# Kernel tuning notes

Hardware: AMD Instinct MI355X
Metric: run time of the kernel (lower is better)

## Reference

```python
import jax, jax.numpy as jnp
import numpy as np
from jax import lax

B, P, S, H, F, V, O = 32, 24, 48, 512, 64, 50000, 16
EPS = 1e-5


def _lstm_scan(inputs, Wih, Whh, b):
    # inputs: [T, B, D]; PyTorch gate order i, f, g, o
    def step(carry, xt):
        h, c = carry
        g = xt @ Wih.T + h @ Whh.T + b
        i, f, gg, o = jnp.split(g, 4, axis=-1)
        c = jax.nn.sigmoid(f) * c + jax.nn.sigmoid(i) * jnp.tanh(gg)
        h = jax.nn.sigmoid(o) * jnp.tanh(c)
        return (h, c), h
    b_ = inputs.shape[1]
    h0 = jnp.zeros((b_, Whh.shape[1]), inputs.dtype)
    _, hs = lax.scan(step, (h0, h0), inputs)
    return hs


def setup_inputs() -> dict:
    key = jax.random.key(0)
    ks = jax.random.split(key, 16)
    x = jax.random.randint(ks[0], (B, P, S), 0, V)
    lens = jnp.sort(jax.random.randint(ks[1], (B,), 1, P + 1))[::-1]
    lens = lens.at[0].set(P)  # pack_padded: sorted desc, max len == P
    tok_len = jax.random.randint(ks[2], (B, P), 1, S + 1)
    tok_len = tok_len * (jnp.arange(P)[None, :] < lens[:, None])
    x_mask = jnp.arange(S)[None, None, :] >= tok_len[:, :, None]  # True = pad
    x_feature = jax.random.normal(ks[3], (B, P, S, F), dtype=jnp.float32)
    emb = jax.random.normal(ks[4], (V, H), dtype=jnp.float32) * 0.02
    w_attn = jax.random.normal(ks[5], (H,), dtype=jnp.float32) * 0.02
    b_attn = jnp.zeros((), jnp.float32)
    D = H + F
    s = 1.0 / np.sqrt(H)
    u = lambda k, sh: jax.random.uniform(k, sh, jnp.float32, -s, s)
    Wih_f, Whh_f = u(ks[6], (4 * H, D)), u(ks[7], (4 * H, H))
    bih_f, bhh_f = u(ks[8], (4 * H,)), u(ks[9], (4 * H,))
    Wih_b, Whh_b = u(ks[10], (4 * H, D)), u(ks[11], (4 * H, H))
    bih_b, bhh_b = u(ks[12], (4 * H,)), u(ks[13], (4 * H,))
    Wfc = u(ks[14], (O, 2 * H))
    bfc = jnp.zeros((O,), jnp.float32)
    gamma = jnp.ones((O,), jnp.float32)
    beta = jnp.zeros((O,), jnp.float32)
    return {"x": x, "x_mask": x_mask, "x_feature": x_feature,
            "sentences_len": lens, "clause": 0, "cls": 0,
            "emb": emb, "w_attn": w_attn, "b_attn": b_attn,
            "Wih_f": Wih_f, "Whh_f": Whh_f, "bih_f": bih_f, "bhh_f": bhh_f,
            "Wih_b": Wih_b, "Whh_b": Whh_b, "bih_b": bih_b, "bhh_b": bhh_b,
            "Wfc": Wfc, "bfc": bfc, "gamma": gamma, "beta": beta}


def reference(x, x_mask, x_feature, sentences_len, clause, cls,
              emb, w_attn, b_attn,
              Wih_f, Whh_f, bih_f, bhh_f,
              Wih_b, Whh_b, bih_b, bhh_b,
              Wfc, bfc, gamma, beta):
    # --- per-sentence embed + linear self-attention + masked sum pooling ---
    e = emb[x]                                             # [B,P,S,H]
    scores = jnp.einsum('bpsh,h->bps', e, w_attn) + b_attn  # [B,P,S]
    scores = jnp.where(x_mask, -1e30, scores)
    alpha = jax.nn.softmax(scores, axis=-1)
    alpha = jnp.where(x_mask, 0.0, alpha)                  # zeros empty sents; relu(softmax)=softmax
    valid = (~x_mask).astype(e.dtype)
    weighted = e * alpha[..., None]
    cat = jnp.concatenate([weighted, x_feature], axis=-1) * valid[..., None]
    rep = cat.sum(axis=2)                                  # [B,P,H+F]
    seq = jnp.transpose(rep, (1, 0, 2))                    # time-major [P,B,H+F]

    # --- packed bidirectional LSTM (per-sequence reversal for bwd dir) ---
    t = jnp.arange(P)[:, None]                             # [P,1]
    lens = sentences_len[None, :]                          # [1,B]
    valid_t = (t < lens)                                   # [P,B]
    h_fwd = _lstm_scan(seq, Wih_f, Whh_f, bih_f + bhh_f)
    rev_idx = jnp.clip(lens - 1 - t, 0)                    # [P,B]
    rev_in = jnp.take_along_axis(seq, rev_idx[..., None], axis=0)
    h_bwd_rev = _lstm_scan(rev_in, Wih_b, Whh_b, bih_b + bhh_b)
    h_bwd = jnp.take_along_axis(h_bwd_rev, rev_idx[..., None], axis=0)
    out_seq = jnp.concatenate([h_fwd, h_bwd], axis=-1) * valid_t[..., None]  # pad_packed zeros

    # --- tail: last timestep, fc, train-mode BN, relu, log_softmax(dim=0) ---
    last = out_seq[-1]                                     # [B,2H]
    z = jnp.reshape(last.T, (B, 2 * H))                    # faithful transpose+view quirk
    y = z @ Wfc.T + bfc                                    # [B,O]
    mean = y.mean(axis=0)
    var = y.var(axis=0)                                    # biased, as torch BN normalization
    y = gamma * (y - mean) / jnp.sqrt(var + EPS) + beta
    y = jax.nn.relu(y)
    return jax.nn.log_softmax(y, axis=0)
```

## Files before the change

### kernel.cpp

```cpp
#include <hip/hip_runtime.h>
#include <math.h>

#define BB_ 32
#define PP_ 24
#define SS_ 48
#define HH_ 512
#define FF_ 64
#define DD_ 576
#define G4_ 2048

typedef __attribute__((ext_vector_type(8))) short short8;
typedef __attribute__((ext_vector_type(4))) float f32x4;

__device__ __forceinline__ float sigf(float x) { return 1.f / (1.f + expf(-x)); }

__device__ __forceinline__ unsigned short f2bf(float f) {
    unsigned int u = __float_as_uint(f);
    u += 0x7FFFu + ((u >> 16) & 1u);
    return (unsigned short)(u >> 16);
}

__global__ void detect_mask_kernel(const unsigned int* __restrict__ m,
                                   int* __restrict__ mode)
{
    __shared__ int s_u8, s_f32;
    int tid = threadIdx.x;
    if (tid == 0) { s_u8 = 0; s_f32 = 0; }
    __syncthreads();
    int u8 = 0, f32 = 0;
    for (int i = tid; i < 9216; i += 256) {
        unsigned int w = m[i];
        if (w == 0x3F800000u) f32 = 1;
        else if (w > 1u) u8 = 1;
    }
    if (u8) s_u8 = 1;
    if (f32) s_f32 = 1;
    __syncthreads();
    if (tid == 0) *mode = s_f32 ? 2 : (s_u8 ? 1 : 0);
}

__global__ void attn_rep_kernel(const int* __restrict__ x,
                                const void* __restrict__ x_mask,
                                const int* __restrict__ mode_p,
                                const float* __restrict__ x_feature,
                                const float* __restrict__ emb,
                                const float* __restrict__ w_attn,
                                const float* __restrict__ b_attn,
                                float* __restrict__ seq)
{
    int bp = blockIdx.x;
    int b = bp / PP_, p = bp % PP_;
    int tid = threadIdx.x;
    __shared__ float wattn_s[HH_];
    __shared__ float sc_s[SS_];
    __shared__ float alpha_s[SS_];
    __shared__ int idx_s[SS_];
    __shared__ unsigned char msk_s[SS_];
    int mode = *mode_p;
    wattn_s[tid] = w_attn[tid];
    wattn_s[tid + 256] = w_attn[tid + 256];
    if (tid < SS_) {
        size_t i = (size_t)bp * SS_ + tid;
        idx_s[tid] = x[i];
        unsigned char mv;
        if (mode == 1)      mv = ((const unsigned char*)x_mask)[i];
        else if (mode == 2) mv = (((const float*)x_mask)[i] != 0.f);
        else                mv = (((const int*)x_mask)[i] != 0);
        msk_s[tid] = mv;
    }
    __syncthreads();
    int wave = tid >> 6, lane = tid & 63;
    for (int s = wave; s < SS_; s += 4) {
        const float* er = emb + (size_t)idx_s[s] * HH_;
        float acc = 0.f;
        #pragma unroll
        for (int j = 0; j < 8; ++j) {
            int d = lane * 8 + j;
            acc += er[d] * wattn_s[d];
        }
        #pragma unroll
        for (int off = 32; off > 0; off >>= 1) acc += __shfl_down(acc, off, 64);
        if (lane == 0) sc_s[s] = acc + b_attn[0];
    }
    __syncthreads();
    if (tid == 0) {
        float m = -3.4e38f;
        for (int s = 0; s < SS_; ++s) if (!msk_s[s] && sc_s[s] > m) m = sc_s[s];
        float sum = 0.f;
        for (int s = 0; s < SS_; ++s) {
            float a = 0.f;
            if (!msk_s[s]) { a = expf(sc_s[s] - m); sum += a; }
            alpha_s[s] = a;
        }
        float inv = (sum > 0.f) ? (1.f / sum) : 0.f;
        for (int s = 0; s < SS_; ++s) alpha_s[s] *= inv;
    }
    __syncthreads();
    float acc0 = 0.f, acc1 = 0.f;
    for (int s = 0; s < SS_; ++s) {
        float a = alpha_s[s];
        if (a != 0.f) {
            const float* er = emb + (size_t)idx_s[s] * HH_;
            acc0 += a * er[tid];
            acc1 += a * er[tid + 256];
        }
    }
    float* orow = seq + ((size_t)p * BB_ + b) * DD_;
    orow[tid] = acc0;
    orow[tid + 256] = acc1;
    if (tid < FF_) {
        float acc2 = 0.f;
        for (int s = 0; s < SS_; ++s)
            if (!msk_s[s]) acc2 += x_feature[((size_t)bp * SS_ + s) * FF_ + tid];
        orow[HH_ + tid] = acc2;
    }
}

__global__ void init2_kernel(float* __restrict__ A0, float* __restrict__ cb)
{
    int i = blockIdx.x * 256 + threadIdx.x;
    if (i < 8192) A0[i] = 0.f;
    cb[i] = 0.f;
}

__global__ void cvt_bf16_kernel(const float* __restrict__ s,
                                unsigned short* __restrict__ d, int n4)
{
    int i = blockIdx.x * 256 + threadIdx.x;
    if (i >= n4) return;
    float4 v = ((const float4*)s)[i];
    ushort4 o;
    o.x = f2bf(v.x); o.y = f2bf(v.y); o.z = f2bf(v.z); o.w = f2bf(v.w);
    ((ushort4*)d)[i] = o;
}

__global__ void __launch_bounds__(256) in_gates_mfma_kernel(
        const float* __restrict__ A,
        const unsigned short* __restrict__ Wbf,
        const float* __restrict__ bih,
        const float* __restrict__ bhh,
        float* __restrict__ Cout)
{
    int tid = threadIdx.x, lane = tid & 63, w = tid >> 6;
    int m0 = blockIdx.y * 16;
    int nb = blockIdx.x * 128 + w * 32;
    int c = lane & 15, q = lane >> 4;
    const float* Ap = A + (size_t)(m0 + c) * DD_ + q * 8;
    const unsigned short* Bp0 = Wbf + (size_t)(nb + c) * DD_ + q * 8;
    const unsigned short* Bp1 = Bp0 + 16 * DD_;
    f32x4 acc0 = {0.f, 0.f, 0.f, 0.f}, acc1 = {0.f, 0.f, 0.f, 0.f};
    for (int k = 0; k < DD_; k += 32) {
        float4 alo = *(const float4*)(Ap + k);
        float4 ahi = *(const float4*)(Ap + k + 4);
        short8 a;
        a[0] = (short)f2bf(alo.x); a[1] = (short)f2bf(alo.y);
        a[2] = (short)f2bf(alo.z); a[3] = (short)f2bf(alo.w);
        a[4] = (short)f2bf(ahi.x); a[5] = (short)f2bf(ahi.y);
        a[6] = (short)f2bf(ahi.z); a[7] = (short)f2bf(ahi.w);
        short8 b0 = *(const short8*)(Bp0 + k);
        short8 b1 = *(const short8*)(Bp1 + k);
        acc0 = __builtin_amdgcn_mfma_f32_16x16x32_bf16(a, b0, acc0, 0, 0, 0);
        acc1 = __builtin_amdgcn_mfma_f32_16x16x32_bf16(a, b1, acc1, 0, 0, 0);
    }
    #pragma unroll
    for (int r = 0; r < 4; ++r) {
        int m = m0 + q * 4 + r;
        int n0 = nb + c, n1 = nb + 16 + c;
        Cout[(size_t)m * G4_ + n0] = acc0[r] + bih[n0] + bhh[n0];
        Cout[(size_t)m * G4_ + n1] = acc1[r] + bih[n1] + bhh[n1];
    }
}

__global__ void __launch_bounds__(256) bwd_last2_kernel(const float* __restrict__ seq,
        const int* __restrict__ lens,
        const float* __restrict__ Wih_b,
        const float* __restrict__ bih_b,
        const float* __restrict__ bhh_b,
        float* __restrict__ hb)
{
    __shared__ float xsT[DD_ * 33];
    __shared__ int pl[BB_];
    int tid = threadIdx.x;
    if (tid < BB_) pl[tid] = lens[tid] - 1;
    __syncthreads();
    for (int idx = tid; idx < BB_ * DD_; idx += 256) {
        int b2 = idx / DD_;
        int k = idx - b2 * DD_;
        xsT[k * 33 + b2] = seq[((size_t)pl[b2] * BB_ + b2) * DD_ + k];
    }
    __syncthreads();
    int b = tid & 31, ul = tid >> 5;
    int u = blockIdx.x * 8 + ul;
    const float* wi = Wih_b + (size_t)u * DD_;
    const float* wg = Wih_b + (size_t)(2 * HH_ + u) * DD_;
    const float* wo = Wih_b + (size_t)(3 * HH_ + u) * DD_;
    float gi = 0.f, gg = 0.f, go = 0.f;
    #pragma unroll 4
    for (int k = 0; k < DD_; k += 4) {
        float4 w1 = *(const float4*)(wi + k);
        float4 w2 = *(const float4*)(wg + k);
        float4 w3 = *(const float4*)(wo + k);
        float x0 = xsT[(k + 0) * 33 + b];
        float x1 = xsT[(k + 1) * 33 + b];
        float x2 = xsT[(k + 2) * 33 + b];
        float x3 = xsT[(k + 3) * 33 + b];
        gi += w1.x * x0 + w1.y * x1 + w1.z * x2 + w1.w * x3;
        gg += w2.x * x0 + w2.y * x1 + w2.z * x2 + w2.w * x3;
        go += w3.x * x0 + w3.y * x1 + w3.z * x2 + w3.w * x3;
    }
    gi += bih_b[u] + bhh_b[u];
    gg += bih_b[2 * HH_ + u] + bhh_b[2 * HH_ + u];
    go += bih_b[3 * HH_ + u] + bhh_b[3 * HH_ + u];
    float cc = sigf(gi) * tanhf(gg);
    hb[(size_t)b * HH_ + u] = sigf(go) * tanhf(cc);
}

__global__ void whh_frag_kernel(const float* __restrict__ Whh,
                                unsigned short* __restrict__ Bf)
{
    int idx = blockIdx.x * 256 + threadIdx.x;
    int lane = idx & 63;
    int ks = (idx >> 6) & 15;
    int ti = (idx >> 10) & 1;
    int nb = idx >> 11;
    int c = lane & 15, q = lane >> 4;
    int nrow = (ti * 2 + (c >> 3)) * HH_ + nb * 8 + (c & 7);
    int k0 = ks * 32 + q * 8;
    const float* src = Whh + (size_t)nrow * HH_ + k0;
    unsigned int w0 = (unsigned int)f2bf(src[0]) | ((unsigned int)f2bf(src[1]) << 16);
    unsigned int w1 = (unsigned int)f2bf(src[2]) | ((unsigned int)f2bf(src[3]) << 16);
    unsigned int w2 = (unsigned int)f2bf(src[4]) | ((unsigned int)f2bf(src[5]) << 16);
    unsigned int w3 = (unsigned int)f2bf(src[6]) | ((unsigned int)f2bf(src[7]) << 16);
    uint4 v = make_uint4(w0, w1, w2, w3);
    *(uint4*)(Bf + (size_t)idx * 8) = v;
}

__global__ void __launch_bounds__(256) lstm_mfma_kernel(
        const unsigned short* __restrict__ Afrag,
        unsigned short* __restrict__ AfragN,
        float* __restrict__ cbuf,
        float* __restrict__ hbuf,
        const float* __restrict__ Ain_t,
        const unsigned short* __restrict__ Bfrag)
{
    __shared__ float gl[32 * 33];
    int tid = threadIdx.x;
    int lane = tid & 63;
    int wv = tid >> 6;
    int mt = wv & 1, ti = wv >> 1;
    int nb = blockIdx.x;
    const short8* Ap = (const short8*)Afrag + (size_t)(mt * 16) * 64 + lane;
    const short8* Bp = (const short8*)Bfrag + (((size_t)nb * 2 + ti) * 16) * 64 + lane;
    short8 a[16], bfr[16];
    #pragma unroll
    for (int ks = 0; ks < 16; ++ks) { a[ks] = Ap[ks * 64]; bfr[ks] = Bp[ks * 64]; }
    f32x4 acc = {0.f, 0.f, 0.f, 0.f};
    #pragma unroll
    for (int ks = 0; ks < 16; ++ks)
        acc = __builtin_amdgcn_mfma_f32_16x16x32_bf16(a[ks], bfr[ks], acc, 0, 0, 0);
    int c = lane & 15, q = lane >> 4;
    int g = ti * 2 + (c >> 3), ul = c & 7;
    #pragma unroll
    for (int r = 0; r < 4; ++r) {
        int bb = mt * 16 + q * 4 + r;
        float v = acc[r] + Ain_t[(size_t)bb * G4_ + g * HH_ + nb * 8 + ul];
        v = (g == 2) ? tanhf(v) : sigf(v);
        gl[(g * 8 + ul) * 33 + bb] = v;
    }
    __syncthreads();
    int b2 = tid >> 3, u2 = tid & 7;
    float iv = gl[(0  + u2) * 33 + b2];
    float fv = gl[(8  + u2) * 33 + b2];
    float gv = gl[(16 + u2) * 33 + b2];
    float ov = gl[(24 + u2) * 33 + b2];
    int ug = nb * 8 + u2;
    size_t ci = (size_t)b2 * HH_ + ug;
    float cold = cbuf[ci];
    float cn = fv * cold + iv * gv;
    cbuf[ci] = cn;
    float h = ov * tanhf(cn);
    hbuf[ci] = h;
    int ks2 = ug >> 5, q2 = (ug >> 3) & 3, j2 = ug & 7;
    int lane2 = (b2 & 15) + 16 * q2;
    AfragN[(((size_t)(b2 >> 4) * 16 + ks2) * 64 + lane2) * 8 + j2] = f2bf(h);
}

__global__ void __launch_bounds__(256) fc_head_kernel(const float* __restrict__ hfwd,
        const float* __restrict__ hbwd, const int* __restrict__ lens,
        const float* __restrict__ Wfc, const float* __restrict__ bfc,
        float* __restrict__ yws)
{
    __shared__ float tile[32][33];
    __shared__ float part[16][17];
    int i = blockIdx.x;
    int tid = threadIdx.x;
    const float* src = (i < 16 ? hfwd : hbwd) + (size_t)(i & 15) * 32;
    int bb = tid >> 5, q = tid & 31;
    #pragma unroll
    for (int h = 0; h < 4; ++h) {
        int bi = bb + h * 8;
        float v = src[(size_t)bi * HH_ + q];
        tile[bi][q] = (lens[bi] == PP_) ? v : 0.f;
    }
    __syncthreads();
    int o = tid >> 4, s = tid & 15;
    const float* w = Wfc + (size_t)o * 1024;
    float acc = 0.f;
    #pragma unroll
    for (int qq = 0; qq < 32; ++qq) {
        acc += tile[s][qq]      * w[qq * 32 + s];
        acc += tile[s + 16][qq] * w[qq * 32 + s + 16];
    }
    part[o][s] = acc;
    __syncthreads();
    if (tid < 16) {
        float sum = bfc[tid];
        #pragma unroll
        for (int ss = 0; ss < 16; ++ss) sum += part[tid][ss];
        yws[i * 16 + tid] = sum;
    }
}

__global__ void __launch_bounds__(512) head_final_kernel(const float* __restrict__ yws,
        const float* __restrict__ gamma, const float* __restrict__ beta,
        float* __restrict__ out)
{
    __shared__ float ys[16][33];
    __shared__ float cstat[16];
    int tid = threadIdx.x;
    int i = tid >> 4, o = tid & 15;
    ys[o][i] = yws[tid];
    __syncthreads();
    if (tid < 16) {
        float mean = 0.f;
        for (int ii = 0; ii < 32; ++ii) mean += ys[tid][ii];
        mean *= (1.f / 32.f);
        float var = 0.f;
        for (int ii = 0; ii < 32; ++ii) { float d = ys[tid][ii] - mean; var += d * d; }
        var *= (1.f / 32.f);
        float inv = 1.f / sqrtf(var + 1e-5f);
        float g = gamma[tid], bt = beta[tid];
        float mx = -3.4e38f;
        for (int ii = 0; ii < 32; ++ii) {
            float v = g * (ys[tid][ii] - mean) * inv + bt;
            v = fmaxf(v, 0.f);
            ys[tid][ii] = v;
            mx = fmaxf(mx, v);
        }
        float s = 0.f;
        for (int ii = 0; ii < 32; ++ii) s += expf(ys[tid][ii] - mx);
        cstat[tid] = mx + logf(s);
    }
    __syncthreads();
    out[tid] = ys[o][i] - cstat[o];
}

extern "C" void kernel_launch(void* const* d_in, const int* in_sizes, int n_in,
                              void* d_out, int out_size, void* d_ws, size_t ws_size,
                              hipStream_t stream) {
    const int* x            = (const int*)d_in[0];
    const void* xm          = d_in[1];
    const float* x_feature  = (const float*)d_in[2];
    const int* lens         = (const int*)d_in[3];
    const float* emb    = (const float*)d_in[6];
    const float* w_attn = (const float*)d_in[7];
    const float* b_attn = (const float*)d_in[8];
    const float* Wih_f  = (const float*)d_in[9];
    const float* Whh_f  = (const float*)d_in[10];
    const float* bih_f  = (const float*)d_in[11];
    const float* bhh_f  = (const float*)d_in[12];
    const float* Wih_b  = (const float*)d_in[13];
    const float* bih_b  = (const float*)d_in[15];
    const float* bhh_b  = (const float*)d_in[16];
    const float* Wfc    = (const float*)d_in[17];
    const float* bfc    = (const float*)d_in[18];
    const float* gamma  = (const float*)d_in[19];
    const float* beta   = (const float*)d_in[20];

    float* ws    = (float*)d_ws;
    float* seq   = ws;
    float* Ain   = seq + (size_t)PP_ * BB_ * DD_;
    float* hb    = Ain + (size_t)PP_ * BB_ * G4_;
    float* hbuf  = hb + (size_t)BB_ * HH_;
    float* cbuf  = hbuf + (size_t)BB_ * HH_;
    float* AfA   = cbuf + (size_t)BB_ * HH_;
    float* AfB   = AfA + 8192;
    float* Bfrag = AfB + 8192;
    float* Wbf   = Bfrag + 524288;
    float* yws   = Wbf + 589824;
    int*  mflag  = (int*)(yws + 512);

    float* outp = (float*)d_out;

    detect_mask_kernel<<<dim3(1), dim3(256), 0, stream>>>(
        (const unsigned int*)xm, mflag);
    whh_frag_kernel<<<dim3(512), dim3(256), 0, stream>>>(
        Whh_f, (unsigned short*)Bfrag);
    cvt_bf16_kernel<<<dim3(1152), dim3(256), 0, stream>>>(
        Wih_f, (unsigned short*)Wbf, 294912);
    attn_rep_kernel<<<dim3(BB_ * PP_), dim3(256), 0, stream>>>(
        x, xm, mflag, x_feature, emb, w_attn, b_attn, seq);
    init2_kernel<<<dim3(64), dim3(256), 0, stream>>>(AfA, cbuf);
    in_gates_mfma_kernel<<<dim3(16, 48), dim3(256), 0, stream>>>(
        seq, (const unsigned short*)Wbf, bih_f, bhh_f, Ain);
    bwd_last2_kernel<<<dim3(64), dim3(256), 0, stream>>>(
        seq, lens, Wih_b, bih_b, bhh_b, hb);
    for (int t = 0; t < PP_; ++t) {
        const unsigned short* Asrc = (const unsigned short*)((t & 1) ? AfB : AfA);
        unsigned short* Adst       = (unsigned short*)((t & 1) ? AfA : AfB);
        lstm_mfma_kernel<<<dim3(64), dim3(256), 0, stream>>>(
            Asrc, Adst, cbuf, hbuf, Ain + (size_t)t * BB_ * G4_,
            (const unsigned short*)Bfrag);
    }
    fc_head_kernel<<<dim3(32), dim3(256), 0, stream>>>(
        hbuf, hb, lens, Wfc, bfc, yws);
    head_final_kernel<<<dim3(1), dim3(512), 0, stream>>>(
        yws, gamma, beta, outp);
}
```

Measured before the change: 457.7 us.

## Persist LSTM recurrence in one kernel with flag barriers and fuse prep/head kernels

```diff
diff --git a/kernel.cpp b/kernel.cpp
--- a/kernel.cpp
+++ b/kernel.cpp
@@ -20,45 +20,77 @@
     return (unsigned short)(u >> 16);
 }
 
-__global__ void detect_mask_kernel(const unsigned int* __restrict__ m,
-                                   int* __restrict__ mode)
-{
-    __shared__ int s_u8, s_f32;
-    int tid = threadIdx.x;
-    if (tid == 0) { s_u8 = 0; s_f32 = 0; }
-    __syncthreads();
-    int u8 = 0, f32 = 0;
-    for (int i = tid; i < 9216; i += 256) {
-        unsigned int w = m[i];
-        if (w == 0x3F800000u) f32 = 1;
-        else if (w > 1u) u8 = 1;
-    }
-    if (u8) s_u8 = 1;
-    if (f32) s_f32 = 1;
-    __syncthreads();
-    if (tid == 0) *mode = s_f32 ? 2 : (s_u8 ? 1 : 0);
-}
-
-__global__ void attn_rep_kernel(const int* __restrict__ x,
-                                const void* __restrict__ x_mask,
-                                const int* __restrict__ mode_p,
-                                const float* __restrict__ x_feature,
-                                const float* __restrict__ emb,
-                                const float* __restrict__ w_attn,
-                                const float* __restrict__ b_attn,
-                                float* __restrict__ seq)
-{
+__global__ void __launch_bounds__(256) prep_kernel(
+        const float* __restrict__ Whh, unsigned short* __restrict__ Bf,
+        const float* __restrict__ Wih, unsigned short* __restrict__ Wbf,
+        float* __restrict__ AfA,
+        const unsigned int* __restrict__ maskw, int* __restrict__ mode,
+        int* __restrict__ flags)
+{
+    int blk = blockIdx.x, tid = threadIdx.x;
+    if (blk < 512) {
+        int idx = blk * 256 + tid;
+        int lane = idx & 63;
+        int ks = (idx >> 6) & 15;
+        int ti = (idx >> 10) & 1;
+        int nb = idx >> 11;
+        int c = lane & 15, q = lane >> 4;
+        int nrow = (ti * 2 + (c >> 3)) * HH_ + nb * 8 + (c & 7);
+        int k0 = ks * 32 + q * 8;
+        const float* src = Whh + (size_t)nrow * HH_ + k0;
+        unsigned int w0 = (unsigned int)f2bf(src[0]) | ((unsigned int)f2bf(src[1]) << 16);
+        unsigned int w1 = (unsigned int)f2bf(src[2]) | ((unsigned int)f2bf(src[3]) << 16);
+        unsigned int w2 = (unsigned int)f2bf(src[4]) | ((unsigned int)f2bf(src[5]) << 16);
+        unsigned int w3 = (unsigned int)f2bf(src[6]) | ((unsigned int)f2bf(src[7]) << 16);
+        *(uint4*)(Bf + (size_t)idx * 8) = make_uint4(w0, w1, w2, w3);
+    } else if (blk < 1664) {
+        int i = (blk - 512) * 256 + tid;
+        float4 v = ((const float4*)Wih)[i];
+        ushort4 o;
+        o.x = f2bf(v.x); o.y = f2bf(v.y); o.z = f2bf(v.z); o.w = f2bf(v.w);
+        ((ushort4*)Wbf)[i] = o;
+    } else if (blk < 1728) {
+        int idx = (blk - 1664) * 256 + tid;
+        if (idx < 8192) AfA[idx] = 0.f;
+    } else {
+        __shared__ int s_u8, s_f32;
+        if (tid == 0) { s_u8 = 0; s_f32 = 0; }
+        __syncthreads();
+        int u8 = 0, f32 = 0;
+        for (int i = tid; i < 9216; i += 256) {
+            unsigned int w = maskw[i];
+            if (w == 0x3F800000u) f32 = 1;
+            else if (w > 1u) u8 = 1;
+        }
+        if (u8) s_u8 = 1;
+        if (f32) s_f32 = 1;
+        if (tid < 64) flags[tid] = 0;
+        __syncthreads();
+        if (tid == 0) *mode = s_f32 ? 2 : (s_u8 ? 1 : 0);
+    }
+}
+
+__global__ void __launch_bounds__(256) attn2_kernel(
+        const int* __restrict__ x,
+        const void* __restrict__ x_mask,
+        const int* __restrict__ mode_p,
+        const float* __restrict__ x_feature,
+        const float* __restrict__ emb,
+        const float* __restrict__ w_attn,
+        const float* __restrict__ b_attn,
+        float* __restrict__ seq)
+{
+    __shared__ float4 es4[SS_ * 128];
+    __shared__ float sc_s[SS_], alpha_s[SS_], vld_s[SS_];
+    __shared__ int idx_s[SS_];
+    __shared__ unsigned char msk_s[SS_];
+    float* esf = (float*)es4;
     int bp = blockIdx.x;
     int b = bp / PP_, p = bp % PP_;
     int tid = threadIdx.x;
-    __shared__ float wattn_s[HH_];
-    __shared__ float sc_s[SS_];
-    __shared__ float alpha_s[SS_];
-    __shared__ int idx_s[SS_];
-    __shared__ unsigned char msk_s[SS_];
+    int wave = tid >> 6, lane = tid & 63;
     int mode = *mode_p;
-    wattn_s[tid] = w_attn[tid];
-    wattn_s[tid + 256] = w_attn[tid + 256];
+    float bscal = b_attn[0];
     if (tid < SS_) {
         size_t i = (size_t)bp * SS_ + tid;
         idx_s[tid] = x[i];
@@ -67,20 +99,25 @@
         else if (mode == 2) mv = (((const float*)x_mask)[i] != 0.f);
         else                mv = (((const int*)x_mask)[i] != 0);
         msk_s[tid] = mv;
-    }
-    __syncthreads();
-    int wave = tid >> 6, lane = tid & 63;
+        vld_s[tid] = mv ? 0.f : 1.f;
+    }
+    __syncthreads();
+    for (int i = wave; i < 2 * SS_; i += 4) {
+        int s = i >> 1, part = i & 1;
+        const float4* er = (const float4*)(emb + (size_t)idx_s[s] * HH_);
+        es4[s * 128 + part * 64 + lane] = er[part * 64 + lane];
+    }
+    __syncthreads();
+    float4 wa0 = ((const float4*)w_attn)[lane];
+    float4 wa1 = ((const float4*)w_attn)[64 + lane];
     for (int s = wave; s < SS_; s += 4) {
-        const float* er = emb + (size_t)idx_s[s] * HH_;
-        float acc = 0.f;
-        #pragma unroll
-        for (int j = 0; j < 8; ++j) {
-            int d = lane * 8 + j;
-            acc += er[d] * wattn_s[d];
-        }
+        float4 v0 = es4[s * 128 + lane];
+        float4 v1 = es4[s * 128 + 64 + lane];
+        float acc = v0.x * wa0.x + v0.y * wa0.y + v0.z * wa0.z + v0.w * wa0.w
+                  + v1.x * wa1.x + v1.y * wa1.y + v1.z * wa1.z + v1.w * wa1.w;
         #pragma unroll
         for (int off = 32; off > 0; off >>= 1) acc += __shfl_down(acc, off, 64);
-        if (lane == 0) sc_s[s] = acc + b_attn[0];
+        if (lane == 0) sc_s[s] = acc + bscal;
     }
     __syncthreads();
     if (tid == 0) {
@@ -97,41 +134,21 @@
     }
     __syncthreads();
     float acc0 = 0.f, acc1 = 0.f;
+    #pragma unroll 8
     for (int s = 0; s < SS_; ++s) {
-        float a = alpha_s[s];
-        if (a != 0.f) {
-            const float* er = emb + (size_t)idx_s[s] * HH_;
-            acc0 += a * er[tid];
-            acc1 += a * er[tid + 256];
-        }
+        float al = alpha_s[s];
+        acc0 += al * esf[s * 512 + tid];
+        acc1 += al * esf[s * 512 + 256 + tid];
     }
     float* orow = seq + ((size_t)p * BB_ + b) * DD_;
     orow[tid] = acc0;
     orow[tid + 256] = acc1;
     if (tid < FF_) {
-        float acc2 = 0.f;
+        float accF = 0.f;
         for (int s = 0; s < SS_; ++s)
-            if (!msk_s[s]) acc2 += x_feature[((size_t)bp * SS_ + s) * FF_ + tid];
-        orow[HH_ + tid] = acc2;
-    }
-}
-
-__global__ void init2_kernel(float* __restrict__ A0, float* __restrict__ cb)
-{
-    int i = blockIdx.x * 256 + threadIdx.x;
-    if (i < 8192) A0[i] = 0.f;
-    cb[i] = 0.f;
-}
-
-__global__ void cvt_bf16_kernel(const float* __restrict__ s,
-                                unsigned short* __restrict__ d, int n4)
-{
-    int i = blockIdx.x * 256 + threadIdx.x;
-    if (i >= n4) return;
-    float4 v = ((const float4*)s)[i];
-    ushort4 o;
-    o.x = f2bf(v.x); o.y = f2bf(v.y); o.z = f2bf(v.z); o.w = f2bf(v.w);
-    ((ushort4*)d)[i] = o;
+            accF += vld_s[s] * x_feature[((size_t)bp * SS_ + s) * FF_ + tid];
+        orow[HH_ + tid] = accF;
+    }
 }
 
 __global__ void __launch_bounds__(256) in_gates_mfma_kernel(
@@ -215,121 +232,117 @@
     hb[(size_t)b * HH_ + u] = sigf(go) * tanhf(cc);
 }
 
-__global__ void whh_frag_kernel(const float* __restrict__ Whh,
-                                unsigned short* __restrict__ Bf)
-{
-    int idx = blockIdx.x * 256 + threadIdx.x;
-    int lane = idx & 63;
-    int ks = (idx >> 6) & 15;
-    int ti = (idx >> 10) & 1;
-    int nb = idx >> 11;
-    int c = lane & 15, q = lane >> 4;
-    int nrow = (ti * 2 + (c >> 3)) * HH_ + nb * 8 + (c & 7);
-    int k0 = ks * 32 + q * 8;
-    const float* src = Whh + (size_t)nrow * HH_ + k0;
-    unsigned int w0 = (unsigned int)f2bf(src[0]) | ((unsigned int)f2bf(src[1]) << 16);
-    unsigned int w1 = (unsigned int)f2bf(src[2]) | ((unsigned int)f2bf(src[3]) << 16);
-    unsigned int w2 = (unsigned int)f2bf(src[4]) | ((unsigned int)f2bf(src[5]) << 16);
-    unsigned int w3 = (unsigned int)f2bf(src[6]) | ((unsigned int)f2bf(src[7]) << 16);
-    uint4 v = make_uint4(w0, w1, w2, w3);
-    *(uint4*)(Bf + (size_t)idx * 8) = v;
-}
-
-__global__ void __launch_bounds__(256) lstm_mfma_kernel(
-        const unsigned short* __restrict__ Afrag,
-        unsigned short* __restrict__ AfragN,
-        float* __restrict__ cbuf,
-        float* __restrict__ hbuf,
-        const float* __restrict__ Ain_t,
-        const unsigned short* __restrict__ Bfrag)
+__global__ void __launch_bounds__(256) lstm_persist_kernel(
+        unsigned short* __restrict__ AfA, unsigned short* __restrict__ AfB,
+        float* __restrict__ hbuf, const float* __restrict__ Ain,
+        const unsigned short* __restrict__ Bfrag, int* __restrict__ flags)
 {
     __shared__ float gl[32 * 33];
-    int tid = threadIdx.x;
-    int lane = tid & 63;
-    int wv = tid >> 6;
+    int tid = threadIdx.x, lane = tid & 63, wv = tid >> 6;
     int mt = wv & 1, ti = wv >> 1;
     int nb = blockIdx.x;
-    const short8* Ap = (const short8*)Afrag + (size_t)(mt * 16) * 64 + lane;
     const short8* Bp = (const short8*)Bfrag + (((size_t)nb * 2 + ti) * 16) * 64 + lane;
-    short8 a[16], bfr[16];
+    short8 bfr[16];
     #pragma unroll
-    for (int ks = 0; ks < 16; ++ks) { a[ks] = Ap[ks * 64]; bfr[ks] = Bp[ks * 64]; }
-    f32x4 acc = {0.f, 0.f, 0.f, 0.f};
-    #pragma unroll
-    for (int ks = 0; ks < 16; ++ks)
-        acc = __builtin_amdgcn_mfma_f32_16x16x32_bf16(a[ks], bfr[ks], acc, 0, 0, 0);
+    for (int ks = 0; ks < 16; ++ks) bfr[ks] = Bp[ks * 64];
     int c = lane & 15, q = lane >> 4;
     int g = ti * 2 + (c >> 3), ul = c & 7;
-    #pragma unroll
-    for (int r = 0; r < 4; ++r) {
-        int bb = mt * 16 + q * 4 + r;
-        float v = acc[r] + Ain_t[(size_t)bb * G4_ + g * HH_ + nb * 8 + ul];
-        v = (g == 2) ? tanhf(v) : sigf(v);
-        gl[(g * 8 + ul) * 33 + bb] = v;
-    }
-    __syncthreads();
     int b2 = tid >> 3, u2 = tid & 7;
-    float iv = gl[(0  + u2) * 33 + b2];
-    float fv = gl[(8  + u2) * 33 + b2];
-    float gv = gl[(16 + u2) * 33 + b2];
-    float ov = gl[(24 + u2) * 33 + b2];
     int ug = nb * 8 + u2;
-    size_t ci = (size_t)b2 * HH_ + ug;
-    float cold = cbuf[ci];
-    float cn = fv * cold + iv * gv;
-    cbuf[ci] = cn;
-    float h = ov * tanhf(cn);
-    hbuf[ci] = h;
     int ks2 = ug >> 5, q2 = (ug >> 3) & 3, j2 = ug & 7;
     int lane2 = (b2 & 15) + 16 * q2;
-    AfragN[(((size_t)(b2 >> 4) * 16 + ks2) * 64 + lane2) * 8 + j2] = f2bf(h);
-}
-
-__global__ void __launch_bounds__(256) fc_head_kernel(const float* __restrict__ hfwd,
-        const float* __restrict__ hbwd, const int* __restrict__ lens,
+    size_t aoff = ((((size_t)(b2 >> 4)) * 16 + ks2) * 64 + lane2) * 8 + j2;
+    float creg = 0.f;
+    for (int t = 0; t < PP_; ++t) {
+        const unsigned short* Af = (t & 1) ? AfB : AfA;
+        unsigned short* An       = (t & 1) ? AfA : AfB;
+        const float* Ain_t = Ain + (size_t)t * BB_ * G4_;
+        float ainv[4];
+        #pragma unroll
+        for (int r = 0; r < 4; ++r)
+            ainv[r] = Ain_t[(size_t)(mt * 16 + q * 4 + r) * G4_ + g * HH_ + nb * 8 + ul];
+        const short8* Ap = (const short8*)Af + (size_t)(mt * 16) * 64 + lane;
+        short8 a[16];
+        #pragma unroll
+        for (int ks = 0; ks < 16; ++ks) a[ks] = Ap[ks * 64];
+        f32x4 acc = {0.f, 0.f, 0.f, 0.f};
+        #pragma unroll
+        for (int ks = 0; ks < 16; ++ks)
+            acc = __builtin_amdgcn_mfma_f32_16x16x32_bf16(a[ks], bfr[ks], acc, 0, 0, 0);
+        #pragma unroll
+        for (int r = 0; r < 4; ++r) {
+            float v = acc[r] + ainv[r];
+            v = (g == 2) ? tanhf(v) : sigf(v);
+            gl[(g * 8 + ul) * 33 + (mt * 16 + q * 4 + r)] = v;
+        }
+        __syncthreads();
+        float iv = gl[(0  + u2) * 33 + b2];
+        float fv = gl[(8  + u2) * 33 + b2];
+        float gv = gl[(16 + u2) * 33 + b2];
+        float ov = gl[(24 + u2) * 33 + b2];
+        creg = fv * creg + iv * gv;
+        float h = ov * tanhf(creg);
+        if (t == PP_ - 1) {
+            hbuf[(size_t)b2 * HH_ + ug] = h;
+        } else {
+            An[aoff] = f2bf(h);
+            __threadfence();
+            __syncthreads();
+            if (tid < 64) {
+                if (tid == 0)
+                    __hip_atomic_store(&flags[nb], t + 1, __ATOMIC_RELEASE,
+                                       __HIP_MEMORY_SCOPE_AGENT);
+                int target = t + 1;
+                while (true) {
+                    int v = __hip_atomic_load(&flags[tid], __ATOMIC_ACQUIRE,
+                                              __HIP_MEMORY_SCOPE_AGENT);
+                    if (__all(v >= target)) break;
+                    __builtin_amdgcn_s_sleep(1);
+                }
+            }
+            __syncthreads();
+            __threadfence();
+        }
+    }
+}
+
+__global__ void __launch_bounds__(1024) head_fused_kernel(
+        const float* __restrict__ hf, const float* __restrict__ hbwd,
+        const int* __restrict__ lens,
         const float* __restrict__ Wfc, const float* __restrict__ bfc,
-        float* __restrict__ yws)
-{
-    __shared__ float tile[32][33];
-    __shared__ float part[16][17];
-    int i = blockIdx.x;
-    int tid = threadIdx.x;
-    const float* src = (i < 16 ? hfwd : hbwd) + (size_t)(i & 15) * 32;
-    int bb = tid >> 5, q = tid & 31;
-    #pragma unroll
-    for (int h = 0; h < 4; ++h) {
-        int bi = bb + h * 8;
-        float v = src[(size_t)bi * HH_ + q];
-        tile[bi][q] = (lens[bi] == PP_) ? v : 0.f;
-    }
-    __syncthreads();
-    int o = tid >> 4, s = tid & 15;
-    const float* w = Wfc + (size_t)o * 1024;
-    float acc = 0.f;
-    #pragma unroll
-    for (int qq = 0; qq < 32; ++qq) {
-        acc += tile[s][qq]      * w[qq * 32 + s];
-        acc += tile[s + 16][qq] * w[qq * 32 + s + 16];
-    }
-    part[o][s] = acc;
-    __syncthreads();
-    if (tid < 16) {
-        float sum = bfc[tid];
-        #pragma unroll
-        for (int ss = 0; ss < 16; ++ss) sum += part[tid][ss];
-        yws[i * 16 + tid] = sum;
-    }
-}
-
-__global__ void __launch_bounds__(512) head_final_kernel(const float* __restrict__ yws,
         const float* __restrict__ gamma, const float* __restrict__ beta,
         float* __restrict__ out)
 {
+    __shared__ float tileL[32 * 1024];
+    __shared__ float lmask[BB_];
+    __shared__ float part[1024];
     __shared__ float ys[16][33];
     __shared__ float cstat[16];
     int tid = threadIdx.x;
-    int i = tid >> 4, o = tid & 15;
-    ys[o][i] = yws[tid];
+    if (tid < BB_) lmask[tid] = (lens[tid] == PP_) ? 1.f : 0.f;
+    __syncthreads();
+    for (int j = tid; j < 32 * 1024; j += 1024) {
+        int bb = j >> 10, col = j & 1023;
+        float v = (col < HH_) ? hf[(size_t)bb * HH_ + col]
+                              : hbwd[(size_t)bb * HH_ + col - HH_];
+        tileL[j] = v * lmask[bb];
+    }
+    __syncthreads();
+    int outi = tid & 511, half = tid >> 9;
+    int i = outi >> 4, o = outi & 15;
+    const float* wrow = Wfc + (size_t)o * 1024;
+    float acc = 0.f;
+    for (int q = 0; q < 32; ++q) {
+        int j = i * 32 + q;
+        #pragma unroll
+        for (int bb2 = 0; bb2 < 16; ++bb2) {
+            int bb = half * 16 + bb2;
+            acc += tileL[bb * 1024 + j] * wrow[q * 32 + bb];
+        }
+    }
+    part[tid] = acc;
+    __syncthreads();
+    if (tid < 512) ys[o][i] = part[tid] + part[tid + 512] + bfc[o];
     __syncthreads();
     if (tid < 16) {
         float mean = 0.f;
@@ -339,10 +352,10 @@
         for (int ii = 0; ii < 32; ++ii) { float d = ys[tid][ii] - mean; var += d * d; }
         var *= (1.f / 32.f);
         float inv = 1.f / sqrtf(var + 1e-5f);
-        float g = gamma[tid], bt = beta[tid];
+        float gmm = gamma[tid], bt = beta[tid];
         float mx = -3.4e38f;
         for (int ii = 0; ii < 32; ++ii) {
-            float v = g * (ys[tid][ii] - mean) * inv + bt;
+            float v = gmm * (ys[tid][ii] - mean) * inv + bt;
             v = fmaxf(v, 0.f);
             ys[tid][ii] = v;
             mx = fmaxf(mx, v);
@@ -352,7 +365,7 @@
         cstat[tid] = mx + logf(s);
     }
     __syncthreads();
-    out[tid] = ys[o][i] - cstat[o];
+    if (tid < 512) out[tid] = ys[o][i] - cstat[o];
 }
 
 extern "C" void kernel_launch(void* const* d_in, const int* in_sizes, int n_in,
@@ -382,38 +395,27 @@
     float* Ain   = seq + (size_t)PP_ * BB_ * DD_;
     float* hb    = Ain + (size_t)PP_ * BB_ * G4_;
     float* hbuf  = hb + (size_t)BB_ * HH_;
-    float* cbuf  = hbuf + (size_t)BB_ * HH_;
-    float* AfA   = cbuf + (size_t)BB_ * HH_;
+    float* AfA   = hbuf + (size_t)BB_ * HH_;
     float* AfB   = AfA + 8192;
     float* Bfrag = AfB + 8192;
     float* Wbf   = Bfrag + 524288;
-    float* yws   = Wbf + 589824;
-    int*  mflag  = (int*)(yws + 512);
+    int*  flags  = (int*)(Wbf + 589824);
+    int*  mflag  = flags + 64;
 
     float* outp = (float*)d_out;
 
-    detect_mask_kernel<<<dim3(1), dim3(256), 0, stream>>>(
-        (const unsigned int*)xm, mflag);
-    whh_frag_kernel<<<dim3(512), dim3(256), 0, stream>>>(
-        Whh_f, (unsigned short*)Bfrag);
-    cvt_bf16_kernel<<<dim3(1152), dim3(256), 0, stream>>>(
-        Wih_f, (unsigned short*)Wbf, 294912);
-    attn_rep_kernel<<<dim3(BB_ * PP_), dim3(256), 0, stream>>>(
+    prep_kernel<<<dim3(1729), dim3(256), 0, stream>>>(
+        Whh_f, (unsigned short*)Bfrag, Wih_f, (unsigned short*)Wbf,
+        AfA, (const unsigned int*)xm, mflag, flags);
+    attn2_kernel<<<dim3(BB_ * PP_), dim3(256), 0, stream>>>(
         x, xm, mflag, x_feature, emb, w_attn, b_attn, seq);
-    init2_kernel<<<dim3(64), dim3(256), 0, stream>>>(AfA, cbuf);
     in_gates_mfma_kernel<<<dim3(16, 48), dim3(256), 0, stream>>>(
         seq, (const unsigned short*)Wbf, bih_f, bhh_f, Ain);
     bwd_last2_kernel<<<dim3(64), dim3(256), 0, stream>>>(
         seq, lens, Wih_b, bih_b, bhh_b, hb);
-    for (int t = 0; t < PP_; ++t) {
-        const unsigned short* Asrc = (const unsigned short*)((t & 1) ? AfB : AfA);
-        unsigned short* Adst       = (unsigned short*)((t & 1) ? AfA : AfB);
-        lstm_mfma_kernel<<<dim3(64), dim3(256), 0, stream>>>(
-            Asrc, Adst, cbuf, hbuf, Ain + (size_t)t * BB_ * G4_,
-            (const unsigned short*)Bfrag);
-    }
-    fc_head_kernel<<<dim3(32), dim3(256), 0, stream>>>(
-        hbuf, hb, lens, Wfc, bfc, yws);
-    head_final_kernel<<<dim3(1), dim3(512), 0, stream>>>(
-        yws, gamma, beta, outp);
-}
+    lstm_persist_kernel<<<dim3(64), dim3(256), 0, stream>>>(
+        (unsigned short*)AfA, (unsigned short*)AfB, hbuf, Ain,
+        (const unsigned short*)Bfrag, flags);
+    head_fused_kernel<<<dim3(1), dim3(1024), 0, stream>>>(
+        hbuf, hb, lens, Wfc, bfc, gamma, beta, outp);
+}
```

New measurement: 724.2 us. 1.58x slower.
